# Performance work log

Measured on AMD Instinct MI355X. Metric: run time of the kernel, lower is better.

## Reference

```python
import jax, jax.numpy as jnp
import numpy as np

ALPHA = 0.2


def setup_inputs() -> dict:
    key = jax.random.key(0)
    k1, k2, k3, k4, k5 = jax.random.split(key, 5)
    N, E, F, C = 100000, 3200000, 512, 64
    in_feat = jax.random.normal(k1, (N, F), dtype=jnp.float32)
    src = jax.random.randint(k2, (E,), 0, N, dtype=jnp.int64)
    dst = jax.random.randint(k3, (E,), 0, N, dtype=jnp.int64)
    # nn.Linear(in_feats, num_classes) params
    bound = 1.0 / np.sqrt(F)
    W = jax.random.uniform(k4, (C, F), dtype=jnp.float32, minval=-bound, maxval=bound)
    b = jax.random.uniform(k5, (C,), dtype=jnp.float32, minval=-bound, maxval=bound)
    return {"in_feat": in_feat, "W": W, "b": b, "src": src, "dst": dst}


def reference(in_feat, W, b, src, dst):
    N = in_feat.shape[0]
    E = src.shape[0]
    # Linear projection: [N, F] @ [F, C] + [C]
    h0 = in_feat @ W.T + b  # [N, C]
    # Symmetric normalization as in DGL APPNPConv (degrees clamped to >= 1)
    ones_e = jnp.ones((E,), dtype=h0.dtype)
    deg_out = jax.ops.segment_sum(ones_e, src, num_segments=N)
    deg_in = jax.ops.segment_sum(ones_e, dst, num_segments=N)
    norm_src = jax.lax.rsqrt(jnp.clip(deg_out, 1.0))  # D_out^{-1/2}
    norm_dst = jax.lax.rsqrt(jnp.clip(deg_in, 1.0))   # D_in^{-1/2}
    # One propagation step (k=1): gather -> scatter-add -> normalize
    msgs = (h0 * norm_src[:, None])[src]               # [E, C]
    agg = jax.ops.segment_sum(msgs, dst, num_segments=N) * norm_dst[:, None]
    # Teleport blend
    h = (1.0 - ALPHA) * agg + ALPHA * h0
    return h
```

## Files before the change

kernel.cpp:

```cpp
#include <hip/hip_runtime.h>

#define N_NODES 100000
#define E_EDGES 3200000
#define F_IN    512
#define C_OUT   64
#define NB      391
#define CAP     10240
#define TILE    16384
#define NTILE   196

typedef __bf16 bf16x8 __attribute__((ext_vector_type(8)));
typedef float  f32x4  __attribute__((ext_vector_type(4)));
typedef float  f32x2  __attribute__((ext_vector_type(2)));

static __device__ __forceinline__ unsigned short f2bf(float f) {
    unsigned int u = __float_as_uint(f);
    u = (u + 0x7FFFu + ((u >> 16) & 1u)) >> 16;
    return (unsigned short)u;
}
static __device__ __forceinline__ float bf2f(unsigned short b) {
    return __uint_as_float(((unsigned int)b) << 16);
}
static __device__ __forceinline__ unsigned char f32_to_fp8(float v) {
    return (unsigned char)(__builtin_amdgcn_cvt_pk_fp8_f32(v, v, 0, false) & 0xFF);
}
static __device__ __forceinline__ f32x2 fp8x2_to_f32(unsigned short u) {
    return __builtin_amdgcn_cvt_pk_f32_fp8((int)(unsigned int)u, false);
}

__global__ __launch_bounds__(512) void zero_kernel(int* __restrict__ cursor_d,
                                                   int* __restrict__ cursor_s) {
    int idx = threadIdx.x;
    if (idx < NB) { cursor_d[idx] = 0; cursor_s[idx] = 0; }
}

__global__ __launch_bounds__(512) void p2_part(const int* __restrict__ src,
                                               const int* __restrict__ dst,
                                               int* __restrict__ cursor_d,
                                               int* __restrict__ cursor_s,
                                               unsigned int* __restrict__ tmp,
                                               unsigned char* __restrict__ tmp2) {
    __shared__ int cd[NB];
    __shared__ int bd[NB];
    __shared__ int cs[NB];
    __shared__ int bs[NB];
    int t = threadIdx.x;
    for (int j = t; j < NB; j += 512) { cd[j] = 0; cs[j] = 0; }
    __syncthreads();
    int tb = blockIdx.x * TILE;
    #pragma unroll 4
    for (int i = 0; i < 32; ++i) {
        int e = tb + i * 512 + t;
        if (e < E_EDGES) {
            atomicAdd(&cd[dst[e] >> 8], 1);
            atomicAdd(&cs[src[e] >> 8], 1);
        }
    }
    __syncthreads();
    for (int j = t; j < NB; j += 512) {
        int c = cd[j];
        bd[j] = j * CAP + (c ? atomicAdd(&cursor_d[j], c) : 0);
        cd[j] = 0;
        c = cs[j];
        bs[j] = j * CAP + (c ? atomicAdd(&cursor_s[j], c) : 0);
        cs[j] = 0;
    }
    __syncthreads();
    #pragma unroll 4
    for (int i = 0; i < 32; ++i) {
        int e = tb + i * 512 + t;
        if (e < E_EDGES) {
            int s = src[e], d = dst[e];
            int db = d >> 8;
            int p = atomicAdd(&cd[db], 1);
            tmp[bd[db] + p] = ((unsigned int)(d & 255) << 24) | (unsigned int)s;
            int sb = s >> 8;
            int q = atomicAdd(&cs[sb], 1);
            tmp2[bs[sb] + q] = (unsigned char)(s & 255);
        }
    }
}

__global__ __launch_bounds__(256) void p3_build(const unsigned int* __restrict__ tmp,
                                                const unsigned char* __restrict__ tmp2,
                                                const int* __restrict__ cursor_d,
                                                const int* __restrict__ cursor_s,
                                                int* __restrict__ row_beg,
                                                int* __restrict__ row_end,
                                                int* __restrict__ edge_src,
                                                float* __restrict__ norm_src,
                                                float* __restrict__ norm_dst) {
    __shared__ int cnt[256];
    __shared__ int off[256];
    __shared__ int lc[256];
    __shared__ int s[256];
    __shared__ int cnt2[256];
    int t = threadIdx.x;
    int b = blockIdx.x;
    int bbase = b * CAP;
    int bend  = bbase + cursor_d[b];
    int sbase = b * CAP;
    int send  = sbase + cursor_s[b];
    cnt[t] = 0;
    lc[t] = 0;
    cnt2[t] = 0;
    __syncthreads();
    for (int e = bbase + t; e < bend; e += 256)
        atomicAdd(&cnt[tmp[e] >> 24], 1);
    for (int e = sbase + t; e < send; e += 256)
        atomicAdd(&cnt2[tmp2[e]], 1);
    __syncthreads();
    int vv = cnt[t];
    s[t] = vv;
    __syncthreads();
    #pragma unroll
    for (int o = 1; o < 256; o <<= 1) {
        int add = (t >= o) ? s[t - o] : 0;
        __syncthreads();
        s[t] += add;
        __syncthreads();
    }
    off[t] = s[t] - vv;
    __syncthreads();
    int node = b * 256 + t;
    if (node < N_NODES) {
        row_beg[node] = bbase + off[t];
        row_end[node] = bbase + off[t] + vv;
        norm_dst[node] = rsqrtf((float)(vv < 1 ? 1 : vv));
        int dg = cnt2[t];
        norm_src[node] = rsqrtf((float)(dg < 1 ? 1 : dg));
    }
    for (int e = bbase + t; e < bend; e += 256) {
        unsigned int v = tmp[e];
        int dl = v >> 24;
        int p = atomicAdd(&lc[dl], 1);
        edge_src[bbase + off[dl] + p] = (int)(v & 0x00FFFFFFu);
    }
}

__global__ __launch_bounds__(256) void gemm_kernel(const float* __restrict__ A,
                                                   const float* __restrict__ W,
                                                   const float* __restrict__ bias,
                                                   const float* __restrict__ norm_src,
                                                   unsigned short* __restrict__ h0b,
                                                   unsigned char* __restrict__ h8) {
    __shared__ unsigned short Wl[64 * 520];

    const int tid  = threadIdx.x;
    const int w    = tid >> 6;
    const int lane = tid & 63;
    const int cl   = lane & 15;
    const int quad = lane >> 4;
    const int row0 = blockIdx.x * 64;

    #pragma unroll 8
    for (int j = 0; j < 32; ++j) {
        int e4 = (j * 256 + tid) * 4;
        float4 wv = *reinterpret_cast<const float4*>(&W[e4]);
        int c = e4 >> 9;
        int k = e4 & 511;
        unsigned short* d = &Wl[c * 520 + k];
        d[0] = f2bf(wv.x); d[1] = f2bf(wv.y); d[2] = f2bf(wv.z); d[3] = f2bf(wv.w);
    }
    __syncthreads();

    int arow = row0 + w * 16 + cl;
    if (arow >= N_NODES) arow = N_NODES - 1;
    const float* aptr = A + (size_t)arow * F_IN + quad * 8;

    f32x4 acc0 = {0.f, 0.f, 0.f, 0.f};
    f32x4 acc1 = {0.f, 0.f, 0.f, 0.f};
    f32x4 acc2 = {0.f, 0.f, 0.f, 0.f};
    f32x4 acc3 = {0.f, 0.f, 0.f, 0.f};

    for (int k0 = 0; k0 < F_IN; k0 += 32) {
        float4 p = *reinterpret_cast<const float4*>(aptr + k0);
        float4 q = *reinterpret_cast<const float4*>(aptr + k0 + 4);
        bf16x8 af;
        af[0] = (__bf16)p.x; af[1] = (__bf16)p.y; af[2] = (__bf16)p.z; af[3] = (__bf16)p.w;
        af[4] = (__bf16)q.x; af[5] = (__bf16)q.y; af[6] = (__bf16)q.z; af[7] = (__bf16)q.w;

        const unsigned short* wb = &Wl[k0 + quad * 8];
        bf16x8 b0 = *reinterpret_cast<const bf16x8*>(wb + (cl +  0) * 520);
        bf16x8 b1 = *reinterpret_cast<const bf16x8*>(wb + (cl + 16) * 520);
        bf16x8 b2 = *reinterpret_cast<const bf16x8*>(wb + (cl + 32) * 520);
        bf16x8 b3 = *reinterpret_cast<const bf16x8*>(wb + (cl + 48) * 520);

        acc0 = __builtin_amdgcn_mfma_f32_16x16x32_bf16(af, b0, acc0, 0, 0, 0);
        acc1 = __builtin_amdgcn_mfma_f32_16x16x32_bf16(af, b1, acc1, 0, 0, 0);
        acc2 = __builtin_amdgcn_mfma_f32_16x16x32_bf16(af, b2, acc2, 0, 0, 0);
        acc3 = __builtin_amdgcn_mfma_f32_16x16x32_bf16(af, b3, acc3, 0, 0, 0);
    }

    float bias0 = bias[cl +  0];
    float bias1 = bias[cl + 16];
    float bias2 = bias[cl + 32];
    float bias3 = bias[cl + 48];
    #pragma unroll
    for (int r = 0; r < 4; ++r) {
        int row = row0 + w * 16 + quad * 4 + r;
        if (row < N_NODES) {
            float v0 = acc0[r] + bias0;
            float v1 = acc1[r] + bias1;
            float v2 = acc2[r] + bias2;
            float v3 = acc3[r] + bias3;
            unsigned short* o = &h0b[(size_t)row * C_OUT + cl];
            o[ 0] = f2bf(v0);
            o[16] = f2bf(v1);
            o[32] = f2bf(v2);
            o[48] = f2bf(v3);
            float ns = norm_src[row];
            unsigned char* o8 = &h8[(size_t)row * C_OUT + cl];
            o8[ 0] = f32_to_fp8(v0 * ns);
            o8[16] = f32_to_fp8(v1 * ns);
            o8[32] = f32_to_fp8(v2 * ns);
            o8[48] = f32_to_fp8(v3 * ns);
        }
    }
}

__global__ __launch_bounds__(256) void gather_kernel(const int* __restrict__ row_beg,
                                                     const int* __restrict__ row_end,
                                                     const int* __restrict__ edge_src,
                                                     const unsigned char* __restrict__ h8,
                                                     const unsigned short* __restrict__ h0b,
                                                     const float* __restrict__ norm_dst,
                                                     float* __restrict__ out) {
    int node = blockIdx.x * 4 + (threadIdx.x >> 6);
    int lane = threadIdx.x & 63;
    if (node >= N_NODES) return;
    int half = lane >> 5;
    int c2   = lane & 31;

    const unsigned short* h8p = reinterpret_cast<const unsigned short*>(h8);
    const unsigned int*   h32 = reinterpret_cast<const unsigned int*>(h0b);

    int beg = row_beg[node];
    int end = row_end[node];
    float ax = 0.0f, ay = 0.0f;

    int base = beg;
    for (; base + 16 <= end; base += 16) {
        int e0 = base + half;
        int s0 = edge_src[e0 +  0];
        int s1 = edge_src[e0 +  2];
        int s2 = edge_src[e0 +  4];
        int s3 = edge_src[e0 +  6];
        int s4 = edge_src[e0 +  8];
        int s5 = edge_src[e0 + 10];
        int s6 = edge_src[e0 + 12];
        int s7 = edge_src[e0 + 14];
        unsigned short u0 = h8p[s0 * 32 + c2];
        unsigned short u1 = h8p[s1 * 32 + c2];
        unsigned short u2 = h8p[s2 * 32 + c2];
        unsigned short u3 = h8p[s3 * 32 + c2];
        unsigned short u4 = h8p[s4 * 32 + c2];
        unsigned short u5 = h8p[s5 * 32 + c2];
        unsigned short u6 = h8p[s6 * 32 + c2];
        unsigned short u7 = h8p[s7 * 32 + c2];
        f32x2 f0 = fp8x2_to_f32(u0);
        f32x2 f1 = fp8x2_to_f32(u1);
        f32x2 f2 = fp8x2_to_f32(u2);
        f32x2 f3 = fp8x2_to_f32(u3);
        f32x2 f4 = fp8x2_to_f32(u4);
        f32x2 f5 = fp8x2_to_f32(u5);
        f32x2 f6 = fp8x2_to_f32(u6);
        f32x2 f7 = fp8x2_to_f32(u7);
        ax += (f0[0] + f1[0]) + (f2[0] + f3[0]) + (f4[0] + f5[0]) + (f6[0] + f7[0]);
        ay += (f0[1] + f1[1]) + (f2[1] + f3[1]) + (f4[1] + f5[1]) + (f6[1] + f7[1]);
    }
    for (int e = base + half; e < end; e += 2) {
        int s = edge_src[e];
        f32x2 f = fp8x2_to_f32(h8p[s * 32 + c2]);
        ax += f[0];
        ay += f[1];
    }

    ax += __shfl(ax, lane ^ 32, 64);
    ay += __shfl(ay, lane ^ 32, 64);

    if (half == 0) {
        unsigned int hu = h32[node * 32 + c2];
        float nd = norm_dst[node];
        float2 r;
        r.x = 0.8f * nd * ax + 0.2f * bf2f((unsigned short)hu);
        r.y = 0.8f * nd * ay + 0.2f * bf2f((unsigned short)(hu >> 16));
        *reinterpret_cast<float2*>(&out[node * C_OUT + c2 * 2]) = r;
    }
}

extern "C" void kernel_launch(void* const* d_in, const int* in_sizes, int n_in,
                              void* d_out, int out_size, void* d_ws, size_t ws_size,
                              hipStream_t stream) {
    const float* in_feat = (const float*)d_in[0];
    const float* W       = (const float*)d_in[1];
    const float* bias    = (const float*)d_in[2];
    const int*   src     = (const int*)d_in[3];
    const int*   dst     = (const int*)d_in[4];
    float* out = (float*)d_out;

    char* p = (char*)d_ws;
    unsigned short* h0b = (unsigned short*)p;  p += (size_t)N_NODES * C_OUT * 2;
    unsigned char*  h8  = (unsigned char*)p;   p += (size_t)N_NODES * C_OUT;
    unsigned int*   tmp = (unsigned int*)p;    p += (size_t)NB * CAP * 4;
    unsigned char*  tmp2= (unsigned char*)p;   p += (size_t)NB * CAP;
    int*   edge_src = (int*)p;                 p += (size_t)NB * CAP * 4;
    int*   row_beg  = (int*)p;                 p += (size_t)N_NODES * 4;
    int*   row_end  = (int*)p;                 p += (size_t)N_NODES * 4;
    float* norm_src = (float*)p;               p += (size_t)N_NODES * 4;
    float* norm_dst = (float*)p;               p += (size_t)N_NODES * 4;
    int*   cursor_d = (int*)p;                 p += (size_t)NB * 4;
    int*   cursor_s = (int*)p;

    zero_kernel<<<1, 512, 0, stream>>>(cursor_d, cursor_s);
    p2_part<<<NTILE, 512, 0, stream>>>(src, dst, cursor_d, cursor_s, tmp, tmp2);
    p3_build<<<NB, 256, 0, stream>>>(tmp, tmp2, cursor_d, cursor_s, row_beg,
                                     row_end, edge_src, norm_src, norm_dst);
    gemm_kernel<<<(N_NODES + 63) / 64, 256, 0, stream>>>(in_feat, W, bias,
                                                         norm_src, h0b, h8);
    gather_kernel<<<(N_NODES + 3) / 4, 256, 0, stream>>>(row_beg, row_end,
                                                         edge_src, h8, h0b,
                                                         norm_dst, out);
}
```

Measured before the change: 505.8 us.

## Replace CSR build and per-node gather with bucket-local LDS atomic aggregation

Removes the per-bucket sort that built a CSR edge list (edge_src, row_beg/row_end). The aggregation kernel now reads the coarse dst-bucketed edge list directly. Each block owns half a bucket (128 nodes), accumulates fp8 source features into a shared-memory float tile with LDS atomics, and counts in-degree on the fly. It also halves the partition tile size so twice as many blocks run. In exchange, every edge bucket is read twice (once per half-block), LDS float atomics may contend on hub nodes, and the summation order is no longer deterministic.

```diff
diff --git a/kernel.cpp b/kernel.cpp
--- a/kernel.cpp
+++ b/kernel.cpp
@@ -6,8 +6,8 @@
 #define C_OUT   64
 #define NB      391
 #define CAP     10240
-#define TILE    16384
-#define NTILE   196
+#define TILE    8192
+#define NTILE   391
 
 typedef __bf16 bf16x8 __attribute__((ext_vector_type(8)));
 typedef float  f32x4  __attribute__((ext_vector_type(4)));
@@ -34,7 +34,7 @@
     if (idx < NB) { cursor_d[idx] = 0; cursor_s[idx] = 0; }
 }
 
-__global__ __launch_bounds__(512) void p2_part(const int* __restrict__ src,
+__global__ __launch_bounds__(256) void p2_part(const int* __restrict__ src,
                                                const int* __restrict__ dst,
                                                int* __restrict__ cursor_d,
                                                int* __restrict__ cursor_s,
@@ -45,19 +45,19 @@
     __shared__ int cs[NB];
     __shared__ int bs[NB];
     int t = threadIdx.x;
-    for (int j = t; j < NB; j += 512) { cd[j] = 0; cs[j] = 0; }
+    for (int j = t; j < NB; j += 256) { cd[j] = 0; cs[j] = 0; }
     __syncthreads();
     int tb = blockIdx.x * TILE;
     #pragma unroll 4
     for (int i = 0; i < 32; ++i) {
-        int e = tb + i * 512 + t;
+        int e = tb + i * 256 + t;
         if (e < E_EDGES) {
             atomicAdd(&cd[dst[e] >> 8], 1);
             atomicAdd(&cs[src[e] >> 8], 1);
         }
     }
     __syncthreads();
-    for (int j = t; j < NB; j += 512) {
+    for (int j = t; j < NB; j += 256) {
         int c = cd[j];
         bd[j] = j * CAP + (c ? atomicAdd(&cursor_d[j], c) : 0);
         cd[j] = 0;
@@ -68,7 +68,7 @@
     __syncthreads();
     #pragma unroll 4
     for (int i = 0; i < 32; ++i) {
-        int e = tb + i * 512 + t;
+        int e = tb + i * 256 + t;
         if (e < E_EDGES) {
             int s = src[e], d = dst[e];
             int db = d >> 8;
@@ -81,60 +81,23 @@
     }
 }
 
-__global__ __launch_bounds__(256) void p3_build(const unsigned int* __restrict__ tmp,
-                                                const unsigned char* __restrict__ tmp2,
-                                                const int* __restrict__ cursor_d,
-                                                const int* __restrict__ cursor_s,
-                                                int* __restrict__ row_beg,
-                                                int* __restrict__ row_end,
-                                                int* __restrict__ edge_src,
-                                                float* __restrict__ norm_src,
-                                                float* __restrict__ norm_dst) {
-    __shared__ int cnt[256];
-    __shared__ int off[256];
-    __shared__ int lc[256];
-    __shared__ int s[256];
+__global__ __launch_bounds__(256) void p3_norm(const unsigned char* __restrict__ tmp2,
+                                               const int* __restrict__ cursor_s,
+                                               float* __restrict__ norm_src) {
     __shared__ int cnt2[256];
     int t = threadIdx.x;
     int b = blockIdx.x;
-    int bbase = b * CAP;
-    int bend  = bbase + cursor_d[b];
+    cnt2[t] = 0;
+    __syncthreads();
     int sbase = b * CAP;
     int send  = sbase + cursor_s[b];
-    cnt[t] = 0;
-    lc[t] = 0;
-    cnt2[t] = 0;
-    __syncthreads();
-    for (int e = bbase + t; e < bend; e += 256)
-        atomicAdd(&cnt[tmp[e] >> 24], 1);
     for (int e = sbase + t; e < send; e += 256)
         atomicAdd(&cnt2[tmp2[e]], 1);
     __syncthreads();
-    int vv = cnt[t];
-    s[t] = vv;
-    __syncthreads();
-    #pragma unroll
-    for (int o = 1; o < 256; o <<= 1) {
-        int add = (t >= o) ? s[t - o] : 0;
-        __syncthreads();
-        s[t] += add;
-        __syncthreads();
-    }
-    off[t] = s[t] - vv;
-    __syncthreads();
     int node = b * 256 + t;
     if (node < N_NODES) {
-        row_beg[node] = bbase + off[t];
-        row_end[node] = bbase + off[t] + vv;
-        norm_dst[node] = rsqrtf((float)(vv < 1 ? 1 : vv));
         int dg = cnt2[t];
         norm_src[node] = rsqrtf((float)(dg < 1 ? 1 : dg));
-    }
-    for (int e = bbase + t; e < bend; e += 256) {
-        unsigned int v = tmp[e];
-        int dl = v >> 24;
-        int p = atomicAdd(&lc[dl], 1);
-        edge_src[bbase + off[dl] + p] = (int)(v & 0x00FFFFFFu);
     }
 }
 
@@ -219,73 +182,81 @@
     }
 }
 
-__global__ __launch_bounds__(256) void gather_kernel(const int* __restrict__ row_beg,
-                                                     const int* __restrict__ row_end,
-                                                     const int* __restrict__ edge_src,
+__global__ __launch_bounds__(512) void gather_bucket(const unsigned int* __restrict__ tmp,
+                                                     const int* __restrict__ cursor_d,
                                                      const unsigned char* __restrict__ h8,
                                                      const unsigned short* __restrict__ h0b,
-                                                     const float* __restrict__ norm_dst,
                                                      float* __restrict__ out) {
-    int node = blockIdx.x * 4 + (threadIdx.x >> 6);
-    int lane = threadIdx.x & 63;
-    if (node >= N_NODES) return;
-    int half = lane >> 5;
-    int c2   = lane & 31;
+    __shared__ float acc[128 * 64];
+    __shared__ int   cnt[128];
+    int t   = threadIdx.x;
+    int b   = blockIdx.x >> 1;
+    int sub = blockIdx.x & 1;
+    #pragma unroll
+    for (int i = 0; i < 16; ++i) acc[i * 512 + t] = 0.0f;
+    if (t < 128) cnt[t] = 0;
+    __syncthreads();
 
     const unsigned short* h8p = reinterpret_cast<const unsigned short*>(h8);
-    const unsigned int*   h32 = reinterpret_cast<const unsigned int*>(h0b);
-
-    int beg = row_beg[node];
-    int end = row_end[node];
-    float ax = 0.0f, ay = 0.0f;
-
-    int base = beg;
-    for (; base + 16 <= end; base += 16) {
-        int e0 = base + half;
-        int s0 = edge_src[e0 +  0];
-        int s1 = edge_src[e0 +  2];
-        int s2 = edge_src[e0 +  4];
-        int s3 = edge_src[e0 +  6];
-        int s4 = edge_src[e0 +  8];
-        int s5 = edge_src[e0 + 10];
-        int s6 = edge_src[e0 + 12];
-        int s7 = edge_src[e0 + 14];
-        unsigned short u0 = h8p[s0 * 32 + c2];
-        unsigned short u1 = h8p[s1 * 32 + c2];
-        unsigned short u2 = h8p[s2 * 32 + c2];
-        unsigned short u3 = h8p[s3 * 32 + c2];
-        unsigned short u4 = h8p[s4 * 32 + c2];
-        unsigned short u5 = h8p[s5 * 32 + c2];
-        unsigned short u6 = h8p[s6 * 32 + c2];
-        unsigned short u7 = h8p[s7 * 32 + c2];
-        f32x2 f0 = fp8x2_to_f32(u0);
-        f32x2 f1 = fp8x2_to_f32(u1);
-        f32x2 f2 = fp8x2_to_f32(u2);
-        f32x2 f3 = fp8x2_to_f32(u3);
-        f32x2 f4 = fp8x2_to_f32(u4);
-        f32x2 f5 = fp8x2_to_f32(u5);
-        f32x2 f6 = fp8x2_to_f32(u6);
-        f32x2 f7 = fp8x2_to_f32(u7);
-        ax += (f0[0] + f1[0]) + (f2[0] + f3[0]) + (f4[0] + f5[0]) + (f6[0] + f7[0]);
-        ay += (f0[1] + f1[1]) + (f2[1] + f3[1]) + (f4[1] + f5[1]) + (f6[1] + f7[1]);
-    }
-    for (int e = base + half; e < end; e += 2) {
-        int s = edge_src[e];
-        f32x2 f = fp8x2_to_f32(h8p[s * 32 + c2]);
-        ax += f[0];
-        ay += f[1];
-    }
-
-    ax += __shfl(ax, lane ^ 32, 64);
-    ay += __shfl(ay, lane ^ 32, 64);
-
-    if (half == 0) {
-        unsigned int hu = h32[node * 32 + c2];
-        float nd = norm_dst[node];
-        float2 r;
-        r.x = 0.8f * nd * ax + 0.2f * bf2f((unsigned short)hu);
-        r.y = 0.8f * nd * ay + 0.2f * bf2f((unsigned short)(hu >> 16));
-        *reinterpret_cast<float2*>(&out[node * C_OUT + c2 * 2]) = r;
+    int slot = t >> 5;
+    int c2   = t & 31;
+
+    int base = b * CAP;
+    int end  = base + cursor_d[b];
+    int e = base + slot;
+    for (; e + 16 < end; e += 32) {
+        unsigned int v0 = tmp[e];
+        unsigned int v1 = tmp[e + 16];
+        int dl0 = (int)(v0 >> 24), s0 = (int)(v0 & 0x00FFFFFFu);
+        int dl1 = (int)(v1 >> 24), s1 = (int)(v1 & 0x00FFFFFFu);
+        bool m0 = (dl0 >> 7) == sub;
+        bool m1 = (dl1 >> 7) == sub;
+        if (m0) {
+            f32x2 f = fp8x2_to_f32(h8p[s0 * 32 + c2]);
+            int a = (dl0 & 127) * 64 + c2 * 2;
+            atomicAdd(&acc[a], f[0]);
+            atomicAdd(&acc[a + 1], f[1]);
+            if (c2 == 0) atomicAdd(&cnt[dl0 & 127], 1);
+        }
+        if (m1) {
+            f32x2 f = fp8x2_to_f32(h8p[s1 * 32 + c2]);
+            int a = (dl1 & 127) * 64 + c2 * 2;
+            atomicAdd(&acc[a], f[0]);
+            atomicAdd(&acc[a + 1], f[1]);
+            if (c2 == 0) atomicAdd(&cnt[dl1 & 127], 1);
+        }
+    }
+    for (; e < end; e += 16) {
+        unsigned int v = tmp[e];
+        int dl = (int)(v >> 24), s = (int)(v & 0x00FFFFFFu);
+        if ((dl >> 7) == sub) {
+            f32x2 f = fp8x2_to_f32(h8p[s * 32 + c2]);
+            int a = (dl & 127) * 64 + c2 * 2;
+            atomicAdd(&acc[a], f[0]);
+            atomicAdd(&acc[a + 1], f[1]);
+            if (c2 == 0) atomicAdd(&cnt[dl & 127], 1);
+        }
+    }
+    __syncthreads();
+
+    int node0 = b * 256 + sub * 128;
+    #pragma unroll
+    for (int i = t; i < 2048; i += 512) {
+        int dl = i >> 4;
+        int c4 = (i & 15) * 4;
+        int node = node0 + dl;
+        if (node < N_NODES) {
+            int dg = cnt[dl];
+            float nd = 0.8f * rsqrtf((float)(dg < 1 ? 1 : dg));
+            const float* a = &acc[dl * 64 + c4];
+            const unsigned short* h = &h0b[(size_t)node * C_OUT + c4];
+            float4 r;
+            r.x = nd * a[0] + 0.2f * bf2f(h[0]);
+            r.y = nd * a[1] + 0.2f * bf2f(h[1]);
+            r.z = nd * a[2] + 0.2f * bf2f(h[2]);
+            r.w = nd * a[3] + 0.2f * bf2f(h[3]);
+            *reinterpret_cast<float4*>(&out[(size_t)node * C_OUT + c4]) = r;
+        }
     }
 }
 
@@ -304,21 +275,14 @@
     unsigned char*  h8  = (unsigned char*)p;   p += (size_t)N_NODES * C_OUT;
     unsigned int*   tmp = (unsigned int*)p;    p += (size_t)NB * CAP * 4;
     unsigned char*  tmp2= (unsigned char*)p;   p += (size_t)NB * CAP;
-    int*   edge_src = (int*)p;                 p += (size_t)NB * CAP * 4;
-    int*   row_beg  = (int*)p;                 p += (size_t)N_NODES * 4;
-    int*   row_end  = (int*)p;                 p += (size_t)N_NODES * 4;
     float* norm_src = (float*)p;               p += (size_t)N_NODES * 4;
-    float* norm_dst = (float*)p;               p += (size_t)N_NODES * 4;
     int*   cursor_d = (int*)p;                 p += (size_t)NB * 4;
     int*   cursor_s = (int*)p;
 
     zero_kernel<<<1, 512, 0, stream>>>(cursor_d, cursor_s);
-    p2_part<<<NTILE, 512, 0, stream>>>(src, dst, cursor_d, cursor_s, tmp, tmp2);
-    p3_build<<<NB, 256, 0, stream>>>(tmp, tmp2, cursor_d, cursor_s, row_beg,
-                                     row_end, edge_src, norm_src, norm_dst);
+    p2_part<<<NTILE, 256, 0, stream>>>(src, dst, cursor_d, cursor_s, tmp, tmp2);
+    p3_norm<<<NB, 256, 0, stream>>>(tmp2, cursor_s, norm_src);
     gemm_kernel<<<(N_NODES + 63) / 64, 256, 0, stream>>>(in_feat, W, bias,
                                                          norm_src, h0b, h8);
-    gather_kernel<<<(N_NODES + 3) / 4, 256, 0, stream>>>(row_beg, row_end,
-                                                         edge_src, h8, h0b,
-                                                         norm_dst, out);
-}
+    gather_bucket<<<NB * 2, 512, 0, stream>>>(tmp, cursor_d, h8, h0b, out);
+}
```

Result: slower. 1.778 ms (+251.5%).
